# Performance work log

Measured on AMD Instinct MI355X. Metric: run time of the kernel, lower is better.

## Reference

```python
import jax, jax.numpy as jnp
import numpy as np

N_NODES = 50000
N_EDGES = 300000
D_IN = 256
D_OUT = 256


def setup_inputs() -> dict:
    key = jax.random.key(0)
    k1, k2, k3, k4 = jax.random.split(key, 4)
    x = jax.random.normal(k1, (N_NODES, D_IN), dtype=jnp.float32)
    edge_index = jax.random.randint(k2, (2, N_EDGES), 0, N_NODES, dtype=jnp.int64)
    edge_weight = jax.random.uniform(k3, (N_EDGES,), dtype=jnp.float32)
    # nn.Linear(D_IN, D_OUT, bias=False): weight shape [out, in]
    W = jax.random.normal(k4, (D_OUT, D_IN), dtype=jnp.float32) * (1.0 / np.sqrt(D_IN))
    return {"x": x, "edge_index": edge_index, "edge_weight": edge_weight, "W": W}


def reference(x, edge_index, edge_weight, W):
    # x = self.linear(x)  -> [N, D_OUT]
    x_proj = jnp.einsum("nd,od->no", x, W)
    # torch.sparse.mm(A_hat, x_proj): out[dst] += A[dst, src] * x_proj[src]
    dst = edge_index[0]
    src = edge_index[1]
    msgs = edge_weight[:, None] * x_proj[src]  # [E, D_OUT]
    out = jax.ops.segment_sum(msgs, dst, num_segments=N_NODES)
    return out
```

## Files before the change

### kernel.cpp

```cpp
#include <hip/hip_runtime.h>
#include <stdint.h>

#define D 256

typedef __bf16 bf16x8 __attribute__((ext_vector_type(8)));
typedef unsigned short u16x8 __attribute__((ext_vector_type(8)));
typedef float f32x4 __attribute__((ext_vector_type(4)));

static __device__ inline unsigned short f2bf(float f) {
    union { float f; unsigned u; } c; c.f = f;
    unsigned u = c.u + 0x7FFFu + ((c.u >> 16) & 1u);
    return (unsigned short)(u >> 16);
}
static __device__ inline float bf2f(unsigned short h) {
    union { unsigned u; float f; } c; c.u = (unsigned)h << 16;
    return c.f;
}

__global__ void count_kernel(const int* __restrict__ dst, int* __restrict__ cnt, int E) {
    int e = blockIdx.x * blockDim.x + threadIdx.x;
    if (e < E) atomicAdd(&cnt[dst[e]], 1);
}

__global__ __launch_bounds__(1024) void scan_local_kernel(const int* __restrict__ cnt,
        int* __restrict__ exsc, int* __restrict__ bsum, int n) {
    int t = threadIdx.x;
    int idx = blockIdx.x * 1024 + t;
    int v = (idx < n) ? cnt[idx] : 0;
    __shared__ int tmp[1024];
    tmp[t] = v;
    __syncthreads();
    for (int off = 1; off < 1024; off <<= 1) {
        int u = 0;
        if (t >= off) u = tmp[t - off];
        __syncthreads();
        tmp[t] += u;
        __syncthreads();
    }
    if (idx < n) exsc[idx] = tmp[t] - v;
    if (t == 1023) bsum[blockIdx.x] = tmp[t];
}

__global__ __launch_bounds__(1024) void scan_bsum_kernel(int* __restrict__ bsum, int nb) {
    int t = threadIdx.x;
    int v = (t < nb) ? bsum[t] : 0;
    __shared__ int tmp[1024];
    tmp[t] = v;
    __syncthreads();
    for (int off = 1; off < 1024; off <<= 1) {
        int u = 0;
        if (t >= off) u = tmp[t - off];
        __syncthreads();
        tmp[t] += u;
        __syncthreads();
    }
    if (t < nb) bsum[t] = tmp[t] - v;
}

__global__ void scan_finalize_kernel(const int* __restrict__ exsc, const int* __restrict__ bsum,
        int* __restrict__ offs, int* __restrict__ cur, int n, int E) {
    int idx = blockIdx.x * blockDim.x + threadIdx.x;
    if (idx < n) {
        int o = exsc[idx] + bsum[idx >> 10];
        offs[idx] = o;
        cur[idx]  = o;
    }
    if (idx == 0) offs[n] = E;
}

__global__ void fill_kernel(const int* __restrict__ dst, const int* __restrict__ src,
        const float* __restrict__ ew, int* __restrict__ cur,
        int* __restrict__ srcS, float* __restrict__ wS, int E) {
    int e = blockIdx.x * blockDim.x + threadIdx.x;
    if (e < E) {
        int d = dst[e];
        int pos = atomicAdd(&cur[d], 1);
        srcS[pos] = src[e];
        wS[pos]   = ew[e];
    }
}

__global__ __launch_bounds__(256) void gemm_fill_kernel(
        const float* __restrict__ X, const float* __restrict__ Wp,
        unsigned short* __restrict__ xproj, int M, int gemmBlocks,
        const int* __restrict__ dst, const int* __restrict__ src,
        const float* __restrict__ ew, int* __restrict__ cur,
        int* __restrict__ srcS, float* __restrict__ wS, int E) {
    __shared__ u16x8 Asm[4 * 64];
    __shared__ u16x8 Bsm[4 * 256];

    if ((int)blockIdx.x >= gemmBlocks) {
        int e = ((int)blockIdx.x - gemmBlocks) * 256 + threadIdx.x;
        if (e < E) {
            int d = dst[e];
            int pos = atomicAdd(&cur[d], 1);
            srcS[pos] = src[e];
            wS[pos]   = ew[e];
        }
        return;
    }

    int tid  = threadIdx.x;
    int lane = tid & 63;
    int wn   = tid >> 6;
    int m0   = blockIdx.x * 64;

    f32x4 acc[4][4];
#pragma unroll
    for (int i = 0; i < 4; ++i)
#pragma unroll
        for (int j = 0; j < 4; ++j)
            acc[i][j] = (f32x4){0.f, 0.f, 0.f, 0.f};

    int arow = tid >> 2;
    int akc  = tid & 3;
    int grow = m0 + arow; if (grow > M - 1) grow = M - 1;
    const float* aBase = X + (size_t)grow * D + akc * 8;

    int l16 = lane & 15, lq = lane >> 4;

    for (int s = 0; s < 8; ++s) {
        int k0 = s * 32;
        {
            const float4* p = (const float4*)(aBase + k0);
            float4 v0 = p[0], v1 = p[1];
            u16x8 h;
            h[0] = f2bf(v0.x); h[1] = f2bf(v0.y); h[2] = f2bf(v0.z); h[3] = f2bf(v0.w);
            h[4] = f2bf(v1.x); h[5] = f2bf(v1.y); h[6] = f2bf(v1.z); h[7] = f2bf(v1.w);
            Asm[akc * 64 + arow] = h;
        }
#pragma unroll
        for (int j = 0; j < 4; ++j) {
            int n = j * 64 + (tid >> 2);
            const float4* p = (const float4*)(Wp + (size_t)n * D + k0 + akc * 8);
            float4 v0 = p[0], v1 = p[1];
            u16x8 h;
            h[0] = f2bf(v0.x); h[1] = f2bf(v0.y); h[2] = f2bf(v0.z); h[3] = f2bf(v0.w);
            h[4] = f2bf(v1.x); h[5] = f2bf(v1.y); h[6] = f2bf(v1.z); h[7] = f2bf(v1.w);
            Bsm[akc * 256 + n] = h;
        }
        __syncthreads();

        u16x8 af[4], bfr[4];
#pragma unroll
        for (int fm = 0; fm < 4; ++fm) af[fm] = Asm[lq * 64 + fm * 16 + l16];
#pragma unroll
        for (int fn = 0; fn < 4; ++fn) bfr[fn] = Bsm[lq * 256 + wn * 64 + fn * 16 + l16];
#pragma unroll
        for (int fm = 0; fm < 4; ++fm)
#pragma unroll
            for (int fn = 0; fn < 4; ++fn)
                acc[fm][fn] = __builtin_amdgcn_mfma_f32_16x16x32_bf16(
                    __builtin_bit_cast(bf16x8, af[fm]),
                    __builtin_bit_cast(bf16x8, bfr[fn]),
                    acc[fm][fn], 0, 0, 0);
        __syncthreads();
    }

#pragma unroll
    for (int fm = 0; fm < 4; ++fm)
#pragma unroll
        for (int fn = 0; fn < 4; ++fn)
#pragma unroll
            for (int r = 0; r < 4; ++r) {
                int row = m0 + fm * 16 + lq * 4 + r;
                int col = wn * 64 + fn * 16 + l16;
                if (row < M) xproj[(size_t)row * D + col] = f2bf(acc[fm][fn][r]);
            }
}

__global__ __launch_bounds__(256) void aggp_kernel(const ushort4* __restrict__ P,
        const int* __restrict__ offs, const int* __restrict__ srcS,
        const float* __restrict__ wS, float4* __restrict__ out4, int N) {
    int wave = threadIdx.x >> 6;
    int lane = threadIdx.x & 63;
    int node = blockIdx.x * 4 + wave;
    if (node >= N) return;
    int beg = offs[node], end = offs[node + 1];
    float ax = 0.f, ay = 0.f, az = 0.f, aw = 0.f;
    int e = beg;
    for (; e + 3 < end; e += 4) {
        int s0 = srcS[e], s1 = srcS[e + 1], s2 = srcS[e + 2], s3 = srcS[e + 3];
        float w0 = wS[e], w1 = wS[e + 1], w2 = wS[e + 2], w3 = wS[e + 3];
        ushort4 h0 = P[(size_t)s0 * 64 + lane];
        ushort4 h1 = P[(size_t)s1 * 64 + lane];
        ushort4 h2 = P[(size_t)s2 * 64 + lane];
        ushort4 h3 = P[(size_t)s3 * 64 + lane];
        ax += w0 * bf2f(h0.x); ay += w0 * bf2f(h0.y); az += w0 * bf2f(h0.z); aw += w0 * bf2f(h0.w);
        ax += w1 * bf2f(h1.x); ay += w1 * bf2f(h1.y); az += w1 * bf2f(h1.z); aw += w1 * bf2f(h1.w);
        ax += w2 * bf2f(h2.x); ay += w2 * bf2f(h2.y); az += w2 * bf2f(h2.z); aw += w2 * bf2f(h2.w);
        ax += w3 * bf2f(h3.x); ay += w3 * bf2f(h3.y); az += w3 * bf2f(h3.z); aw += w3 * bf2f(h3.w);
    }
    for (; e < end; ++e) {
        int s0 = srcS[e];
        float w0 = wS[e];
        ushort4 h0 = P[(size_t)s0 * 64 + lane];
        ax += w0 * bf2f(h0.x); ay += w0 * bf2f(h0.y); az += w0 * bf2f(h0.z); aw += w0 * bf2f(h0.w);
    }
    float4 r; r.x = ax; r.y = ay; r.z = az; r.w = aw;
    out4[(size_t)node * 64 + lane] = r;
}

__global__ __launch_bounds__(256) void agg_kernel(const float4* __restrict__ X4,
        const int* __restrict__ offs, const int* __restrict__ srcS,
        const float* __restrict__ wS, float4* __restrict__ agg4, int N) {
    int wave = threadIdx.x >> 6;
    int lane = threadIdx.x & 63;
    int node = blockIdx.x * 4 + wave;
    if (node >= N) return;
    int beg = offs[node], end = offs[node + 1];
    float ax = 0.f, ay = 0.f, az = 0.f, aw = 0.f;
    for (int e = beg; e < end; ++e) {
        int sN = srcS[e];
        float wt = wS[e];
        float4 xv = X4[(size_t)sN * 64 + lane];
        ax += wt * xv.x; ay += wt * xv.y; az += wt * xv.z; aw += wt * xv.w;
    }
    float4 r; r.x = ax; r.y = ay; r.z = az; r.w = aw;
    agg4[(size_t)node * 64 + lane] = r;
}

__global__ __launch_bounds__(256) void gemm_kernel(const float* __restrict__ A,
        const float* __restrict__ Wp, float* __restrict__ out, int M) {
    __shared__ u16x8 Asm[4 * 64];
    __shared__ u16x8 Bsm[4 * 256];
    int tid  = threadIdx.x;
    int lane = tid & 63;
    int wn   = tid >> 6;
    int m0   = blockIdx.x * 64;
    f32x4 acc[4][4];
#pragma unroll
    for (int i = 0; i < 4; ++i)
#pragma unroll
        for (int j = 0; j < 4; ++j)
            acc[i][j] = (f32x4){0.f, 0.f, 0.f, 0.f};
    int arow = tid >> 2;
    int akc  = tid & 3;
    int grow = m0 + arow; if (grow > M - 1) grow = M - 1;
    const float* aBase = A + (size_t)grow * D + akc * 8;
    int l16 = lane & 15, lq = lane >> 4;
    for (int s = 0; s < 8; ++s) {
        int k0 = s * 32;
        {
            const float4* p = (const float4*)(aBase + k0);
            float4 v0 = p[0], v1 = p[1];
            u16x8 h;
            h[0] = f2bf(v0.x); h[1] = f2bf(v0.y); h[2] = f2bf(v0.z); h[3] = f2bf(v0.w);
            h[4] = f2bf(v1.x); h[5] = f2bf(v1.y); h[6] = f2bf(v1.z); h[7] = f2bf(v1.w);
            Asm[akc * 64 + arow] = h;
        }
#pragma unroll
        for (int j = 0; j < 4; ++j) {
            int n = j * 64 + (tid >> 2);
            const float4* p = (const float4*)(Wp + (size_t)n * D + k0 + akc * 8);
            float4 v0 = p[0], v1 = p[1];
            u16x8 h;
            h[0] = f2bf(v0.x); h[1] = f2bf(v0.y); h[2] = f2bf(v0.z); h[3] = f2bf(v0.w);
            h[4] = f2bf(v1.x); h[5] = f2bf(v1.y); h[6] = f2bf(v1.z); h[7] = f2bf(v1.w);
            Bsm[akc * 256 + n] = h;
        }
        __syncthreads();
        u16x8 af[4], bfr[4];
#pragma unroll
        for (int fm = 0; fm < 4; ++fm) af[fm] = Asm[lq * 64 + fm * 16 + l16];
#pragma unroll
        for (int fn = 0; fn < 4; ++fn) bfr[fn] = Bsm[lq * 256 + wn * 64 + fn * 16 + l16];
#pragma unroll
        for (int fm = 0; fm < 4; ++fm)
#pragma unroll
            for (int fn = 0; fn < 4; ++fn)
                acc[fm][fn] = __builtin_amdgcn_mfma_f32_16x16x32_bf16(
                    __builtin_bit_cast(bf16x8, af[fm]),
                    __builtin_bit_cast(bf16x8, bfr[fn]),
                    acc[fm][fn], 0, 0, 0);
        __syncthreads();
    }
#pragma unroll
    for (int fm = 0; fm < 4; ++fm)
#pragma unroll
        for (int fn = 0; fn < 4; ++fn)
#pragma unroll
            for (int r = 0; r < 4; ++r) {
                int row = m0 + fm * 16 + lq * 4 + r;
                int col = wn * 64 + fn * 16 + l16;
                if (row < M) out[(size_t)row * D + col] = acc[fm][fn][r];
            }
}

extern "C" void kernel_launch(void* const* d_in, const int* in_sizes, int n_in,
                              void* d_out, int out_size, void* d_ws, size_t ws_size,
                              hipStream_t stream) {
    const float* X  = (const float*)d_in[0];
    const int*   ei = (const int*)d_in[1];
    const float* ew = (const float*)d_in[2];
    const float* Wp = (const float*)d_in[3];
    float* out = (float*)d_out;

    int N = in_sizes[0] / D;
    int E = in_sizes[2];
    const int* dst = ei;
    const int* src = ei + E;
    int nb = (N + 1023) / 1024;

    size_t xpBytes  = (size_t)N * D * sizeof(unsigned short);
    size_t csrInts  = (size_t)4 * N + 1 + nb + 2 * (size_t)E;
    size_t csrBytes = csrInts * sizeof(int);
    bool planB = (ws_size >= xpBytes + csrBytes + 256);

    uint8_t* ws = (uint8_t*)d_ws;
    unsigned short* xproj = (unsigned short*)ws;
    int* csr = planB ? (int*)(ws + ((xpBytes + 255) & ~(size_t)255)) : (int*)ws;

    int* cnt  = csr;
    int* offs = cnt + N;
    int* cur  = offs + N + 1;
    int* srcS = cur + N;
    float* wS = (float*)(srcS + E);
    int* exsc = (int*)(wS + E);
    int* bsum = exsc + N;

    hipMemsetAsync(cnt, 0, (size_t)N * sizeof(int), stream);
    count_kernel<<<dim3((E + 255) / 256), dim3(256), 0, stream>>>(dst, cnt, E);
    scan_local_kernel<<<dim3(nb), dim3(1024), 0, stream>>>(cnt, exsc, bsum, N);
    scan_bsum_kernel<<<dim3(1), dim3(1024), 0, stream>>>(bsum, nb);
    scan_finalize_kernel<<<dim3((N + 255) / 256), dim3(256), 0, stream>>>(exsc, bsum, offs, cur, N, E);

    if (planB) {
        int gemmBlocks = (N + 63) / 64;
        int fillBlocks = (E + 255) / 256;
        gemm_fill_kernel<<<dim3(gemmBlocks + fillBlocks), dim3(256), 0, stream>>>(
            X, Wp, xproj, N, gemmBlocks, dst, src, ew, cur, srcS, wS, E);
        aggp_kernel<<<dim3((N + 3) / 4), dim3(256), 0, stream>>>(
            (const ushort4*)xproj, offs, srcS, wS, (float4*)out, N);
    } else {
        fill_kernel<<<dim3((E + 255) / 256), dim3(256), 0, stream>>>(dst, src, ew, cur, srcS, wS, E);
        agg_kernel<<<dim3((N + 3) / 4), dim3(256), 0, stream>>>((const float4*)X, offs, srcS, wS,
                                                                (float4*)out, N);
        gemm_kernel<<<dim3((N + 63) / 64), dim3(256), 0, stream>>>(out, Wp, out, N);
    }
}
```

Measured before the change: 183.9 us.

## Make projection GEMM persistent with the whole weight matrix staged in LDS

The combined GEMM and CSR-fill kernel becomes a persistent kernel with a fixed grid of 256 blocks of 512 threads. Each block first runs a grid-strided edge-fill loop, then converts all of W to bf16 once into a 128KB LDS buffer laid out in MFMA fragment order. Each wave then works through 16-row chunks, loading X directly into registers. This removes the repeated per-block reloading and conversion of W, along with the per-k-step barriers. The block-sum scan is also replaced by a single-wave shuffle scan. The trade-offs are heavy LDS use that limits occupancy, and the fill now running serially before the GEMM inside each block.

```diff
diff --git a/kernel.cpp b/kernel.cpp
--- a/kernel.cpp
+++ b/kernel.cpp
@@ -41,20 +41,15 @@
     if (t == 1023) bsum[blockIdx.x] = tmp[t];
 }
 
-__global__ __launch_bounds__(1024) void scan_bsum_kernel(int* __restrict__ bsum, int nb) {
+__global__ void scan_bsum_kernel(int* __restrict__ bsum, int nb) {
     int t = threadIdx.x;
-    int v = (t < nb) ? bsum[t] : 0;
-    __shared__ int tmp[1024];
-    tmp[t] = v;
-    __syncthreads();
-    for (int off = 1; off < 1024; off <<= 1) {
-        int u = 0;
-        if (t >= off) u = tmp[t - off];
-        __syncthreads();
-        tmp[t] += u;
-        __syncthreads();
-    }
-    if (t < nb) bsum[t] = tmp[t] - v;
+    int orig = (t < nb) ? bsum[t] : 0;
+    int v = orig;
+    for (int off = 1; off < 64; off <<= 1) {
+        int u = __shfl_up(v, off, 64);
+        if (t >= off) v += u;
+    }
+    if (t < nb) bsum[t] = v - orig;
 }
 
 __global__ void scan_finalize_kernel(const int* __restrict__ exsc, const int* __restrict__ bsum,
@@ -80,93 +75,85 @@
     }
 }
 
-__global__ __launch_bounds__(256) void gemm_fill_kernel(
+__global__ __launch_bounds__(512, 2) void gemmp_kernel(
         const float* __restrict__ X, const float* __restrict__ Wp,
-        unsigned short* __restrict__ xproj, int M, int gemmBlocks,
+        unsigned short* __restrict__ xproj, int M,
         const int* __restrict__ dst, const int* __restrict__ src,
         const float* __restrict__ ew, int* __restrict__ cur,
         int* __restrict__ srcS, float* __restrict__ wS, int E) {
-    __shared__ u16x8 Asm[4 * 64];
-    __shared__ u16x8 Bsm[4 * 256];
-
-    if ((int)blockIdx.x >= gemmBlocks) {
-        int e = ((int)blockIdx.x - gemmBlocks) * 256 + threadIdx.x;
-        if (e < E) {
-            int d = dst[e];
-            int pos = atomicAdd(&cur[d], 1);
-            srcS[pos] = src[e];
-            wS[pos]   = ew[e];
-        }
-        return;
-    }
-
-    int tid  = threadIdx.x;
+    __shared__ u16x8 Wl[16 * 8 * 64];
+
+    int tid = threadIdx.x;
+
+    int stride = (int)gridDim.x * 512;
+    for (int e = (int)blockIdx.x * 512 + tid; e < E; e += stride) {
+        int d = dst[e];
+        int pos = atomicAdd(&cur[d], 1);
+        srcS[pos] = src[e];
+        wS[pos]   = ew[e];
+    }
+
+    for (int f = tid; f < 16 * 8 * 64; f += 512) {
+        int n  = f >> 5;
+        int k0 = (f & 31) << 3;
+        const float4* p = (const float4*)(Wp + (size_t)n * D + k0);
+        float4 v0 = p[0], v1 = p[1];
+        u16x8 h;
+        h[0] = f2bf(v0.x); h[1] = f2bf(v0.y); h[2] = f2bf(v0.z); h[3] = f2bf(v0.w);
+        h[4] = f2bf(v1.x); h[5] = f2bf(v1.y); h[6] = f2bf(v1.z); h[7] = f2bf(v1.w);
+        int t  = n >> 4, l16 = n & 15;
+        int s  = k0 >> 5, lq = (k0 >> 3) & 3;
+        Wl[(t * 8 + s) * 64 + lq * 16 + l16] = h;
+    }
+    __syncthreads();
+
     int lane = tid & 63;
-    int wn   = tid >> 6;
-    int m0   = blockIdx.x * 64;
-
-    f32x4 acc[4][4];
-#pragma unroll
-    for (int i = 0; i < 4; ++i)
-#pragma unroll
-        for (int j = 0; j < 4; ++j)
-            acc[i][j] = (f32x4){0.f, 0.f, 0.f, 0.f};
-
-    int arow = tid >> 2;
-    int akc  = tid & 3;
-    int grow = m0 + arow; if (grow > M - 1) grow = M - 1;
-    const float* aBase = X + (size_t)grow * D + akc * 8;
-
     int l16 = lane & 15, lq = lane >> 4;
-
-    for (int s = 0; s < 8; ++s) {
-        int k0 = s * 32;
-        {
-            const float4* p = (const float4*)(aBase + k0);
+    int wid = (int)blockIdx.x * 8 + (tid >> 6);
+    int nwaves = (int)gridDim.x * 8;
+    int nchunk = (M + 15) >> 4;
+
+    for (int c = wid; c < nchunk; c += nwaves) {
+        int m0 = c << 4;
+        int orow = m0 + l16;
+        int crow = orow > M - 1 ? M - 1 : orow;
+        const float* xb = X + (size_t)crow * D + lq * 8;
+
+        u16x8 xf[8];
+#pragma unroll
+        for (int s = 0; s < 8; ++s) {
+            const float4* p = (const float4*)(xb + s * 32);
             float4 v0 = p[0], v1 = p[1];
             u16x8 h;
             h[0] = f2bf(v0.x); h[1] = f2bf(v0.y); h[2] = f2bf(v0.z); h[3] = f2bf(v0.w);
             h[4] = f2bf(v1.x); h[5] = f2bf(v1.y); h[6] = f2bf(v1.z); h[7] = f2bf(v1.w);
-            Asm[akc * 64 + arow] = h;
+            xf[s] = h;
         }
-#pragma unroll
-        for (int j = 0; j < 4; ++j) {
-            int n = j * 64 + (tid >> 2);
-            const float4* p = (const float4*)(Wp + (size_t)n * D + k0 + akc * 8);
-            float4 v0 = p[0], v1 = p[1];
-            u16x8 h;
-            h[0] = f2bf(v0.x); h[1] = f2bf(v0.y); h[2] = f2bf(v0.z); h[3] = f2bf(v0.w);
-            h[4] = f2bf(v1.x); h[5] = f2bf(v1.y); h[6] = f2bf(v1.z); h[7] = f2bf(v1.w);
-            Bsm[akc * 256 + n] = h;
+
+        f32x4 acc[16];
+#pragma unroll
+        for (int t = 0; t < 16; ++t) acc[t] = (f32x4){0.f, 0.f, 0.f, 0.f};
+
+#pragma unroll
+        for (int t = 0; t < 16; ++t)
+#pragma unroll
+            for (int s = 0; s < 8; ++s)
+                acc[t] = __builtin_amdgcn_mfma_f32_16x16x32_bf16(
+                    __builtin_bit_cast(bf16x8, Wl[(t * 8 + s) * 64 + lane]),
+                    __builtin_bit_cast(bf16x8, xf[s]),
+                    acc[t], 0, 0, 0);
+
+        if (orow < M) {
+            ushort4* op = (ushort4*)(xproj + (size_t)orow * D);
+#pragma unroll
+            for (int t = 0; t < 16; ++t) {
+                ushort4 us;
+                us.x = f2bf(acc[t][0]); us.y = f2bf(acc[t][1]);
+                us.z = f2bf(acc[t][2]); us.w = f2bf(acc[t][3]);
+                op[(t * 16 + lq * 4) >> 2] = us;
+            }
         }
-        __syncthreads();
-
-        u16x8 af[4], bfr[4];
-#pragma unroll
-        for (int fm = 0; fm < 4; ++fm) af[fm] = Asm[lq * 64 + fm * 16 + l16];
-#pragma unroll
-        for (int fn = 0; fn < 4; ++fn) bfr[fn] = Bsm[lq * 256 + wn * 64 + fn * 16 + l16];
-#pragma unroll
-        for (int fm = 0; fm < 4; ++fm)
-#pragma unroll
-            for (int fn = 0; fn < 4; ++fn)
-                acc[fm][fn] = __builtin_amdgcn_mfma_f32_16x16x32_bf16(
-                    __builtin_bit_cast(bf16x8, af[fm]),
-                    __builtin_bit_cast(bf16x8, bfr[fn]),
-                    acc[fm][fn], 0, 0, 0);
-        __syncthreads();
-    }
-
-#pragma unroll
-    for (int fm = 0; fm < 4; ++fm)
-#pragma unroll
-        for (int fn = 0; fn < 4; ++fn)
-#pragma unroll
-            for (int r = 0; r < 4; ++r) {
-                int row = m0 + fm * 16 + lq * 4 + r;
-                int col = wn * 64 + fn * 16 + l16;
-                if (row < M) xproj[(size_t)row * D + col] = f2bf(acc[fm][fn][r]);
-            }
+    }
 }
 
 __global__ __launch_bounds__(256) void aggp_kernel(const ushort4* __restrict__ P,
@@ -322,14 +309,12 @@
     hipMemsetAsync(cnt, 0, (size_t)N * sizeof(int), stream);
     count_kernel<<<dim3((E + 255) / 256), dim3(256), 0, stream>>>(dst, cnt, E);
     scan_local_kernel<<<dim3(nb), dim3(1024), 0, stream>>>(cnt, exsc, bsum, N);
-    scan_bsum_kernel<<<dim3(1), dim3(1024), 0, stream>>>(bsum, nb);
+    scan_bsum_kernel<<<dim3(1), dim3(64), 0, stream>>>(bsum, nb);
     scan_finalize_kernel<<<dim3((N + 255) / 256), dim3(256), 0, stream>>>(exsc, bsum, offs, cur, N, E);
 
     if (planB) {
-        int gemmBlocks = (N + 63) / 64;
-        int fillBlocks = (E + 255) / 256;
-        gemm_fill_kernel<<<dim3(gemmBlocks + fillBlocks), dim3(256), 0, stream>>>(
-            X, Wp, xproj, N, gemmBlocks, dst, src, ew, cur, srcS, wS, E);
+        gemmp_kernel<<<dim3(256), dim3(512), 0, stream>>>(
+            X, Wp, xproj, N, dst, src, ew, cur, srcS, wS, E);
         aggp_kernel<<<dim3((N + 3) / 4), dim3(256), 0, stream>>>(
             (const ushort4*)xproj, offs, srcS, wS, (float4*)out, N);
     } else {
```

New measurement: 340.3 us. 1.85x slower.
